# Kernel optimization log

Hardware: AMD Instinct MI355X
Metric: run time of the kernel (lower is better)

The kernel has to match this reference:

```python
import jax, jax.numpy as jnp
import numpy as np


def _build_transform():
    # Deterministic re-creation of SegmentationAugmentation.build_3d_transform
    # with flip=True, offset=0.1, scale=0.2, rotate=True.
    rng = np.random.default_rng(0)
    t = np.eye(4, dtype=np.float32)
    for i in range(3):
        if rng.random() > 0.5:
            t[i, i] *= -1.0
        t[i, 3] = 0.1 * (rng.random() * 2.0 - 1.0)
        t[i, i] *= 1.0 + 0.2 * (rng.random() * 2.0 - 1.0)
    a = rng.random() * 2.0 * np.pi
    s, c = np.sin(a), np.cos(a)
    rot = np.array([[c, -s, 0, 0], [s, c, 0, 0], [0, 0, 1, 0], [0, 0, 0, 1]],
                   dtype=np.float32)
    return t @ rot


def _affine_grid(theta, size):
    # theta: [B,3,4]; size: (B,C,D,H,W); align_corners=False.
    B, C, D, H, W = size
    def lin(n):
        # pixel-center normalized coords: (2i+1)/n - 1
        return (2.0 * jnp.arange(n, dtype=jnp.float32) + 1.0) / n - 1.0
    z, y, x = jnp.meshgrid(lin(D), lin(H), lin(W), indexing='ij')
    pts = jnp.stack([x, y, z], axis=-1)  # [D,H,W,3], (x,y,z) order as in torch
    return (jnp.einsum('bij,dhwj->bdhwi', theta[:, :, :3], pts)
            + theta[:, None, None, None, :, 3])


def _grid_sample_3d_border(inp, grid):
    # trilinear grid_sample, padding_mode='border', align_corners=False.
    # inp: [B,C,D,H,W]; grid: [B,Do,Ho,Wo,3] with (x,y,z) normalized coords.
    B, C, D, H, W = inp.shape
    Do, Ho, Wo = grid.shape[1:4]

    def unnorm(cn, n):
        # align_corners=False unnormalize, then border clamp
        return jnp.clip(((cn + 1.0) * n - 1.0) * 0.5, 0.0, n - 1.0)

    x = unnorm(grid[..., 0], W)
    y = unnorm(grid[..., 1], H)
    z = unnorm(grid[..., 2], D)
    x0 = jnp.floor(x); y0 = jnp.floor(y); z0 = jnp.floor(z)
    fx, fy, fz = x - x0, y - y0, z - z0
    x0i = x0.astype(jnp.int32); y0i = y0.astype(jnp.int32); z0i = z0.astype(jnp.int32)
    x1i = jnp.minimum(x0i + 1, W - 1)
    y1i = jnp.minimum(y0i + 1, H - 1)
    z1i = jnp.minimum(z0i + 1, D - 1)

    inp_flat = inp.reshape(B, C, D * H * W)
    N = Do * Ho * Wo
    out = jnp.zeros((B, C, N), dtype=inp.dtype)
    for zi, wz in ((z0i, 1.0 - fz), (z1i, fz)):
        for yi, wy in ((y0i, 1.0 - fy), (y1i, fy)):
            for xi, wx in ((x0i, 1.0 - fx), (x1i, fx)):
                idx = ((zi * H + yi) * W + xi).reshape(B, 1, N)
                v = jnp.take_along_axis(
                    inp_flat, jnp.broadcast_to(idx, (B, C, N)), axis=2)
                w = (wz * wy * wx).reshape(B, 1, N)
                out = out + v * w
    return out.reshape(B, C, Do, Ho, Wo)


def setup_inputs() -> dict:
    key = jax.random.key(0)
    k1, k2 = jax.random.split(key)
    input_g = jax.random.normal(k1, (8, 1, 128, 128, 128), dtype=jnp.float32)
    label_g = jax.random.uniform(k2, (8, 1, 128, 128, 128), dtype=jnp.float32)
    transform = jnp.asarray(_build_transform())
    return {"input_g": input_g, "label_g": label_g, "transform": transform}


def reference(input_g, label_g, transform):
    # transpose(-3,-1): swap depth and width axes
    inp = jnp.swapaxes(input_g, -3, -1)
    lab = jnp.swapaxes(label_g, -3, -1)
    B = inp.shape[0]
    theta = jnp.broadcast_to(transform[:3][None], (B, 3, 4)).astype(jnp.float32)
    grid = _affine_grid(theta, inp.shape)
    aug_inp = _grid_sample_3d_border(inp, grid)
    aug_lab = _grid_sample_3d_border(lab, grid)
    aug_inp = jnp.swapaxes(aug_inp, -3, -1)
    aug_lab = jnp.swapaxes(aug_lab, -3, -1)
    return aug_inp, aug_lab > 0.5
```

## Files before the change

kernel.cpp:

```cpp
#include <hip/hip_runtime.h>


#define NV 128
#define TOTAL (8 * NV * NV * NV)

__global__ __launch_bounds__(128) void seg_aug_kernel(
    const float* __restrict__ in,
    const float* __restrict__ lab,
    const float* __restrict__ T,
    float* __restrict__ out_in,
    float* __restrict__ out_lab)
{
#pragma clang fp contract(off)
    const int o4 = threadIdx.x;
    const int o3 = blockIdx.x & (NV - 1);
    const int o2 = (blockIdx.x >> 7) & (NV - 1);
    const int b  = blockIdx.x >> 14;

    float p2 = (2.0f * (float)o2 + 1.0f) / 128.0f - 1.0f;
    float p3 = (2.0f * (float)o3 + 1.0f) / 128.0f - 1.0f;
    float ux = (T[0] * p2 + T[1] * p3) + T[3];
    float uy = (T[4] * p2 + T[5] * p3) + T[7];
    float gx = ((ux + 1.0f) * 128.0f - 1.0f) * 0.5f;
    float gy = ((uy + 1.0f) * 128.0f - 1.0f) * 0.5f;
    gx = fminf(fmaxf(gx, 0.0f), 127.0f);
    gy = fminf(fmaxf(gy, 0.0f), 127.0f);
    float fx0f = floorf(gx), fy0f = floorf(gy);
    float fx = gx - fx0f;
    float fy = gy - fy0f;
    const int ix0 = __builtin_amdgcn_readfirstlane((int)fx0f);
    const int iy0 = __builtin_amdgcn_readfirstlane((int)fy0f);
    const int ix1 = min(ix0 + 1, NV - 1);
    const int iy1 = min(iy0 + 1, NV - 1);
    float wx0 = 1.0f - fx, wx1 = fx;
    float wy0 = 1.0f - fy, wy1 = fy;

    float p4 = (2.0f * (float)o4 + 1.0f) / 128.0f - 1.0f;
    float uz = T[10] * p4 + T[11];
    float gz = ((uz + 1.0f) * 128.0f - 1.0f) * 0.5f;
    gz = fminf(fmaxf(gz, 0.0f), 127.0f);
    float fz0f = floorf(gz);
    float fz = gz - fz0f;
    int iz0 = (int)fz0f;
    int iz1 = min(iz0 + 1, NV - 1);
    float wz0 = 1.0f - fz, wz1 = fz;

    const size_t bbase = (size_t)b << 21;
    const float* ibp = in  + bbase;
    const float* lbp = lab + bbase;
    const int r00 = (ix0 * NV + iy0) * NV;
    const int r01 = (ix0 * NV + iy1) * NV;
    const int r10 = (ix1 * NV + iy0) * NV;
    const int r11 = (ix1 * NV + iy1) * NV;

    float vi_000 = ibp[r00 + iz0];
    float vi_100 = ibp[r10 + iz0];
    float vi_010 = ibp[r01 + iz0];
    float vi_110 = ibp[r11 + iz0];
    float vi_001 = ibp[r00 + iz1];
    float vi_101 = ibp[r10 + iz1];
    float vi_011 = ibp[r01 + iz1];
    float vi_111 = ibp[r11 + iz1];
    float vl_000 = lbp[r00 + iz0];
    float vl_100 = lbp[r10 + iz0];
    float vl_010 = lbp[r01 + iz0];
    float vl_110 = lbp[r11 + iz0];
    float vl_001 = lbp[r00 + iz1];
    float vl_101 = lbp[r10 + iz1];
    float vl_011 = lbp[r01 + iz1];
    float vl_111 = lbp[r11 + iz1];

    float w1 = (wz0 * wy0) * wx0;
    float w2 = (wz0 * wy0) * wx1;
    float w3 = (wz0 * wy1) * wx0;
    float w4 = (wz0 * wy1) * wx1;
    float w5 = (wz1 * wy0) * wx0;
    float w6 = (wz1 * wy0) * wx1;
    float w7 = (wz1 * wy1) * wx0;
    float w8 = (wz1 * wy1) * wx1;

    float acc_i = 0.0f;
    acc_i = acc_i + vi_000 * w1;
    acc_i = acc_i + vi_100 * w2;
    acc_i = acc_i + vi_010 * w3;
    acc_i = acc_i + vi_110 * w4;
    acc_i = acc_i + vi_001 * w5;
    acc_i = acc_i + vi_101 * w6;
    acc_i = acc_i + vi_011 * w7;
    acc_i = acc_i + vi_111 * w8;

    float acc_l = 0.0f;
    acc_l = acc_l + vl_000 * w1;
    acc_l = acc_l + vl_100 * w2;
    acc_l = acc_l + vl_010 * w3;
    acc_l = acc_l + vl_110 * w4;
    acc_l = acc_l + vl_001 * w5;
    acc_l = acc_l + vl_101 * w6;
    acc_l = acc_l + vl_011 * w7;
    acc_l = acc_l + vl_111 * w8;

    const int oidx = blockIdx.x * NV + o4;
    out_in[oidx]  = acc_i;
    out_lab[oidx] = (acc_l > 0.5f) ? 1.0f : 0.0f;
}

extern "C" void kernel_launch(void* const* d_in, const int* in_sizes, int n_in,
                              void* d_out, int out_size, void* d_ws, size_t ws_size,
                              hipStream_t stream) {
    const float* in  = (const float*)d_in[0];
    const float* lab = (const float*)d_in[1];
    const float* T   = (const float*)d_in[2];
    float* out_in  = (float*)d_out;
    float* out_lab = (float*)d_out + TOTAL;

    dim3 grid(TOTAL / 128);
    dim3 block(128);
    seg_aug_kernel<<<grid, block, 0, stream>>>(in, lab, T, out_in, out_lab);
}
```

Measured before the change: 263.1 us.

## Stage the four source rows per block into LDS via direct global-to-LDS loads

Each block now cooperatively copies the four needed 128-float z-rows of both input and label into shared memory using 16-byte global_load_lds transfers, then each thread reads its two z-neighbours from LDS. This replaces sixteen scattered per-thread global gathers with coalesced row loads. In exchange it adds a block barrier, a small LDS footprint, and clamp/select logic to handle the z border.

```diff
diff --git a/kernel.cpp b/kernel.cpp
--- a/kernel.cpp
+++ b/kernel.cpp
@@ -12,7 +12,9 @@
     float* __restrict__ out_lab)
 {
 #pragma clang fp contract(off)
-    const int o4 = threadIdx.x;
+    __shared__ float s[8 * NV];
+
+    const int t  = threadIdx.x;
     const int o3 = blockIdx.x & (NV - 1);
     const int o2 = (blockIdx.x >> 7) & (NV - 1);
     const int b  = blockIdx.x >> 14;
@@ -35,71 +37,84 @@
     float wx0 = 1.0f - fx, wx1 = fx;
     float wy0 = 1.0f - fy, wy1 = fy;
 
-    float p4 = (2.0f * (float)o4 + 1.0f) / 128.0f - 1.0f;
+    const size_t bbase = (size_t)b << 21;
+    const float* ibp = in  + bbase;
+    const float* lbp = lab + bbase;
+    {
+        const int rid = t >> 5;
+        const int seg = t & 31;
+        const int ixS = (rid & 2) ? ix1 : ix0;
+        const int iyS = (rid & 1) ? iy1 : iy0;
+        const int off = (ixS * NV + iyS) * NV + seg * 4;
+        __builtin_amdgcn_global_load_lds(ibp + off, &s[t * 4],       16, 0, 0);
+        __builtin_amdgcn_global_load_lds(lbp + off, &s[512 + t * 4], 16, 0, 0);
+    }
+
+    float p4 = (2.0f * (float)t + 1.0f) / 128.0f - 1.0f;
     float uz = T[10] * p4 + T[11];
     float gz = ((uz + 1.0f) * 128.0f - 1.0f) * 0.5f;
     gz = fminf(fmaxf(gz, 0.0f), 127.0f);
     float fz0f = floorf(gz);
     float fz = gz - fz0f;
     int iz0 = (int)fz0f;
-    int iz1 = min(iz0 + 1, NV - 1);
     float wz0 = 1.0f - fz, wz1 = fz;
 
-    const size_t bbase = (size_t)b << 21;
-    const float* ibp = in  + bbase;
-    const float* lbp = lab + bbase;
-    const int r00 = (ix0 * NV + iy0) * NV;
-    const int r01 = (ix0 * NV + iy1) * NV;
-    const int r10 = (ix1 * NV + iy0) * NV;
-    const int r11 = (ix1 * NV + iy1) * NV;
+    const int zb = min(iz0, NV - 2);
+    const bool hi = (iz0 == NV - 1);
 
-    float vi_000 = ibp[r00 + iz0];
-    float vi_100 = ibp[r10 + iz0];
-    float vi_010 = ibp[r01 + iz0];
-    float vi_110 = ibp[r11 + iz0];
-    float vi_001 = ibp[r00 + iz1];
-    float vi_101 = ibp[r10 + iz1];
-    float vi_011 = ibp[r01 + iz1];
-    float vi_111 = ibp[r11 + iz1];
-    float vl_000 = lbp[r00 + iz0];
-    float vl_100 = lbp[r10 + iz0];
-    float vl_010 = lbp[r01 + iz0];
-    float vl_110 = lbp[r11 + iz0];
-    float vl_001 = lbp[r00 + iz1];
-    float vl_101 = lbp[r10 + iz1];
-    float vl_011 = lbp[r01 + iz1];
-    float vl_111 = lbp[r11 + iz1];
+    __syncthreads();
 
-    float w1 = (wz0 * wy0) * wx0;
-    float w2 = (wz0 * wy0) * wx1;
-    float w3 = (wz0 * wy1) * wx0;
-    float w4 = (wz0 * wy1) * wx1;
-    float w5 = (wz1 * wy0) * wx0;
-    float w6 = (wz1 * wy0) * wx1;
-    float w7 = (wz1 * wy1) * wx0;
-    float w8 = (wz1 * wy1) * wx1;
+    #define PAIR(ROW, A, B) \
+        float A = s[(ROW) * NV + zb]; \
+        float B = s[(ROW) * NV + zb + 1];
+
+    PAIR(0, ia00, ib00)
+    PAIR(1, ia01, ib01)
+    PAIR(2, ia10, ib10)
+    PAIR(3, ia11, ib11)
+    PAIR(4, la00, lb00)
+    PAIR(5, la01, lb01)
+    PAIR(6, la10, lb10)
+    PAIR(7, la11, lb11)
+    #undef PAIR
+
+    float vi000 = hi ? ib00 : ia00;
+    float vi010 = hi ? ib01 : ia01;
+    float vi100 = hi ? ib10 : ia10;
+    float vi110 = hi ? ib11 : ia11;
+    float vl000 = hi ? lb00 : la00;
+    float vl010 = hi ? lb01 : la01;
+    float vl100 = hi ? lb10 : la10;
+    float vl110 = hi ? lb11 : la11;
+
+    float tz0y0 = wz0 * wy0, tz0y1 = wz0 * wy1;
+    float tz1y0 = wz1 * wy0, tz1y1 = wz1 * wy1;
+    float w1 = tz0y0 * wx0, w2 = tz0y0 * wx1;
+    float w3 = tz0y1 * wx0, w4 = tz0y1 * wx1;
+    float w5 = tz1y0 * wx0, w6 = tz1y0 * wx1;
+    float w7 = tz1y1 * wx0, w8 = tz1y1 * wx1;
 
     float acc_i = 0.0f;
-    acc_i = acc_i + vi_000 * w1;
-    acc_i = acc_i + vi_100 * w2;
-    acc_i = acc_i + vi_010 * w3;
-    acc_i = acc_i + vi_110 * w4;
-    acc_i = acc_i + vi_001 * w5;
-    acc_i = acc_i + vi_101 * w6;
-    acc_i = acc_i + vi_011 * w7;
-    acc_i = acc_i + vi_111 * w8;
+    acc_i = acc_i + vi000 * w1;
+    acc_i = acc_i + vi100 * w2;
+    acc_i = acc_i + vi010 * w3;
+    acc_i = acc_i + vi110 * w4;
+    acc_i = acc_i + ib00 * w5;
+    acc_i = acc_i + ib10 * w6;
+    acc_i = acc_i + ib01 * w7;
+    acc_i = acc_i + ib11 * w8;
 
     float acc_l = 0.0f;
-    acc_l = acc_l + vl_000 * w1;
-    acc_l = acc_l + vl_100 * w2;
-    acc_l = acc_l + vl_010 * w3;
-    acc_l = acc_l + vl_110 * w4;
-    acc_l = acc_l + vl_001 * w5;
-    acc_l = acc_l + vl_101 * w6;
-    acc_l = acc_l + vl_011 * w7;
-    acc_l = acc_l + vl_111 * w8;
+    acc_l = acc_l + vl000 * w1;
+    acc_l = acc_l + vl100 * w2;
+    acc_l = acc_l + vl010 * w3;
+    acc_l = acc_l + vl110 * w4;
+    acc_l = acc_l + lb00 * w5;
+    acc_l = acc_l + lb10 * w6;
+    acc_l = acc_l + lb01 * w7;
+    acc_l = acc_l + lb11 * w8;
 
-    const int oidx = blockIdx.x * NV + o4;
+    const int oidx = blockIdx.x * NV + t;
     out_in[oidx]  = acc_i;
     out_lab[oidx] = (acc_l > 0.5f) ? 1.0f : 0.0f;
 }
```

New measurement: 248.1 us. 1.06x faster.
